# Kernel optimization log

Measured on AMD Instinct MI355X. Metric: run time of the kernel, lower is better.

Reference implementation:

```python
import jax, jax.numpy as jnp
import numpy as np

DIM = 2048
N_HEADS = 16
HEAD_DIM = DIM // N_HEADS  # 128
HIDDEN = 8192
EPS = 1e-6
NEG = -1e9


def rmsnorm(x, w):
    xf = x.astype(jnp.float32)
    y = xf * jax.lax.rsqrt(jnp.mean(xf * xf, axis=-1, keepdims=True) + EPS)
    return y.astype(x.dtype) * w


def apply_rope(x, cos, sin):
    # x: [B,S,H,Hd]; cos/sin: [S,Hd//2] -> broadcast [1,S,1,Hd//2]
    xf = x.astype(jnp.float32)
    xr = xf[..., 0::2]
    xi = xf[..., 1::2]
    c = cos[None, :, None, :]
    s = sin[None, :, None, :]
    or_ = xr * c - xi * s
    oi_ = xr * s + xi * c
    out = jnp.stack([or_, oi_], axis=-1).reshape(x.shape)
    return out.astype(x.dtype)


def setup_inputs() -> dict:
    key = jax.random.key(0)
    ks = jax.random.split(key, 10)
    B, S = 1, 2048
    x = jax.random.normal(ks[0], (B, S, DIM), dtype=jnp.float32)
    # RoPE frequencies (Llama-style, theta=10000)
    inv_freq = 1.0 / (10000.0 ** (jnp.arange(0, HEAD_DIM, 2, dtype=jnp.float32) / HEAD_DIM))
    angles = jnp.arange(S, dtype=jnp.float32)[:, None] * inv_freq[None, :]  # [S, Hd//2]
    freqs_cos = jnp.cos(angles)
    freqs_sin = jnp.sin(angles)
    # causal additive mask [1,1,S,S]
    mask = jnp.where(jnp.tril(jnp.ones((S, S), dtype=bool)), 0.0, NEG).astype(jnp.float32)[None, None]
    sc = 0.02
    wq = jax.random.normal(ks[1], (DIM, DIM), dtype=jnp.float32) * sc
    wk = jax.random.normal(ks[2], (DIM, DIM), dtype=jnp.float32) * sc
    wv = jax.random.normal(ks[3], (DIM, DIM), dtype=jnp.float32) * sc
    wo = jax.random.normal(ks[4], (DIM, DIM), dtype=jnp.float32) * sc
    w1 = jax.random.normal(ks[5], (DIM, HIDDEN), dtype=jnp.float32) * sc
    w2 = jax.random.normal(ks[6], (HIDDEN, DIM), dtype=jnp.float32) * sc
    w3 = jax.random.normal(ks[7], (DIM, HIDDEN), dtype=jnp.float32) * sc
    attn_norm_w = jnp.ones((DIM,), dtype=jnp.float32)
    ffn_norm_w = jnp.ones((DIM,), dtype=jnp.float32)
    return {"x": x, "freqs_cos": freqs_cos, "freqs_sin": freqs_sin, "mask": mask,
            "wq": wq, "wk": wk, "wv": wv, "wo": wo, "w1": w1, "w2": w2, "w3": w3,
            "attn_norm_w": attn_norm_w, "ffn_norm_w": ffn_norm_w}


def reference(x, freqs_cos, freqs_sin, mask, wq, wk, wv, wo, w1, w2, w3, attn_norm_w, ffn_norm_w):
    B, S, D = x.shape
    # --- attention (pre-norm) ---
    hn = rmsnorm(x, attn_norm_w)
    q = (hn @ wq).reshape(B, S, N_HEADS, HEAD_DIM)
    k = (hn @ wk).reshape(B, S, N_HEADS, HEAD_DIM)
    v = (hn @ wv).reshape(B, S, N_HEADS, HEAD_DIM)
    q = apply_rope(q, freqs_cos, freqs_sin)
    k = apply_rope(k, freqs_cos, freqs_sin)
    scores = jnp.einsum('bqhd,bkhd->bhqk', q, k) / (HEAD_DIM ** 0.5) + mask
    attn = jax.nn.softmax(scores.astype(jnp.float32), axis=-1).astype(q.dtype)
    ctx = jnp.einsum('bhqk,bkhd->bqhd', attn, v).reshape(B, S, D)
    h = x + ctx @ wo
    # --- SwiGLU FFN (pre-norm) ---
    fn = rmsnorm(h, ffn_norm_w)
    ff = (jax.nn.silu(fn @ w1) * (fn @ w3)) @ w2
    return h + ff
```

## Files before the change

kernel.cpp:

```cpp
#include <hip/hip_runtime.h>
#include <hip/hip_bf16.h>

#define DIM 2048
#define HEAD_DIM 128
#define N_HEADS 16
#define SEQ 2048
#define HID 8192
#define SQKV 6144

typedef short bf16x8 __attribute__((ext_vector_type(8)));
typedef float f32x4 __attribute__((ext_vector_type(4)));
using bf16 = __hip_bfloat16;

#define MFMA16(a, b, c) __builtin_amdgcn_mfma_f32_16x16x32_bf16(a, b, c, 0, 0, 0)

__device__ __forceinline__ unsigned short f2bu(float f) {
    union { bf16 b; unsigned short u; } cv;
    cv.b = __float2bfloat16(f);
    return cv.u;
}
__device__ __forceinline__ float bu2f(unsigned short u) {
    union { unsigned short u; bf16 b; } cv;
    cv.u = u;
    return __bfloat162float(cv.b);
}

__device__ __forceinline__ void gl16(const void* g, void* l) {
    __builtin_amdgcn_global_load_lds(
        (const __attribute__((address_space(1))) unsigned int*)g,
        (__attribute__((address_space(3))) unsigned int*)l, 16, 0, 0);
}

__global__ __launch_bounds__(256) void rmsnorm_bf16_k(
    const float* __restrict__ x, const float* __restrict__ w, bf16* __restrict__ y)
{
    const int row = blockIdx.x;
    const int tid = threadIdx.x;
    const float* xr = x + (size_t)row * DIM;
    float4 v0 = ((const float4*)xr)[tid];
    float4 v1 = ((const float4*)xr)[tid + 256];
    float ss = v0.x*v0.x + v0.y*v0.y + v0.z*v0.z + v0.w*v0.w
             + v1.x*v1.x + v1.y*v1.y + v1.z*v1.z + v1.w*v1.w;
    for (int o = 32; o > 0; o >>= 1) ss += __shfl_down(ss, o);
    __shared__ float red[4];
    if ((tid & 63) == 0) red[tid >> 6] = ss;
    __syncthreads();
    float tot = red[0] + red[1] + red[2] + red[3];
    float r = rsqrtf(tot * (1.0f / DIM) + 1e-6f);
    float4 w0 = ((const float4*)w)[tid];
    float4 w1 = ((const float4*)w)[tid + 256];
    ushort4 o0, o1;
    o0.x = f2bu(v0.x * r * w0.x); o0.y = f2bu(v0.y * r * w0.y);
    o0.z = f2bu(v0.z * r * w0.z); o0.w = f2bu(v0.w * r * w0.w);
    o1.x = f2bu(v1.x * r * w1.x); o1.y = f2bu(v1.y * r * w1.y);
    o1.z = f2bu(v1.z * r * w1.z); o1.w = f2bu(v1.w * r * w1.w);
    ushort4* yr = (ushort4*)(y + (size_t)row * DIM);
    yr[tid] = o0;
    yr[tid + 256] = o1;
}

__global__ __launch_bounds__(256) void rmsnorm4_k(
    const bf16* __restrict__ part, const float* __restrict__ x,
    const float* __restrict__ w, float* __restrict__ hout, bf16* __restrict__ y)
{
    const int row = blockIdx.x;
    const int tid = threadIdx.x;
    const size_t base = (size_t)row * DIM + tid * 8;
    const size_t SP = (size_t)SEQ * DIM;
    float4 a0 = *(const float4*)(x + base);
    float4 a1 = *(const float4*)(x + base + 4);
    bf16x8 p0 = *(const bf16x8*)(part + base);
    bf16x8 p1 = *(const bf16x8*)(part + SP + base);
    bf16x8 p2 = *(const bf16x8*)(part + 2 * SP + base);
    bf16x8 p3 = *(const bf16x8*)(part + 3 * SP + base);
    float r8[8];
    float ss = 0.0f;
#pragma unroll
    for (int e = 0; e < 8; ++e) {
        const float xa = e < 4 ? (&a0.x)[e] : (&a1.x)[e - 4];
        const float v = xa + ((bu2f((unsigned short)p0[e]) + bu2f((unsigned short)p1[e]))
                            + (bu2f((unsigned short)p2[e]) + bu2f((unsigned short)p3[e])));
        r8[e] = v;
        ss += v * v;
    }
    *(float4*)(hout + base)     = make_float4(r8[0], r8[1], r8[2], r8[3]);
    *(float4*)(hout + base + 4) = make_float4(r8[4], r8[5], r8[6], r8[7]);
    for (int o = 32; o > 0; o >>= 1) ss += __shfl_down(ss, o);
    __shared__ float red[4];
    if ((tid & 63) == 0) red[tid >> 6] = ss;
    __syncthreads();
    float tot = red[0] + red[1] + red[2] + red[3];
    float r = rsqrtf(tot * (1.0f / DIM) + 1e-6f);
    float4 w0 = *(const float4*)(w + tid * 8);
    float4 w1 = *(const float4*)(w + tid * 8 + 4);
    bf16x8 o8;
#pragma unroll
    for (int e = 0; e < 8; ++e) {
        const float ww = e < 4 ? (&w0.x)[e] : (&w1.x)[e - 4];
        o8[e] = (short)f2bu(r8[e] * r * ww);
    }
    *(bf16x8*)((unsigned short*)y + base) = o8;
}

__global__ __launch_bounds__(256) void reduce4_k(
    const bf16* __restrict__ part, const float* __restrict__ h, float* __restrict__ out)
{
    const size_t i = ((size_t)blockIdx.x * 256 + threadIdx.x) * 8;
    const size_t SP = (size_t)SEQ * DIM;
    float4 a0 = *(const float4*)(h + i);
    float4 a1 = *(const float4*)(h + i + 4);
    bf16x8 p0 = *(const bf16x8*)(part + i);
    bf16x8 p1 = *(const bf16x8*)(part + SP + i);
    bf16x8 p2 = *(const bf16x8*)(part + 2 * SP + i);
    bf16x8 p3 = *(const bf16x8*)(part + 3 * SP + i);
    float r8[8];
#pragma unroll
    for (int e = 0; e < 8; ++e) {
        const float xa = e < 4 ? (&a0.x)[e] : (&a1.x)[e - 4];
        r8[e] = xa + ((bu2f((unsigned short)p0[e]) + bu2f((unsigned short)p1[e]))
                    + (bu2f((unsigned short)p2[e]) + bu2f((unsigned short)p3[e])));
    }
    *(float4*)(out + i)     = make_float4(r8[0], r8[1], r8[2], r8[3]);
    *(float4*)(out + i + 4) = make_float4(r8[4], r8[5], r8[6], r8[7]);
}

__device__ __forceinline__ void convT64_body(
    const float* __restrict__ in, bf16* __restrict__ out, int R, int C,
    int bx, int by)
{
    __shared__ unsigned short t[64][72];
    const int tid = threadIdx.x;
    const int x0 = bx * 64;
    const int y0 = by * 64;
    const int tx = tid & 15, ty = tid >> 4;
#pragma unroll
    for (int i = 0; i < 4; ++i) {
        const int row = ty + i * 16;
        float4 v = *(const float4*)(in + (size_t)(y0 + row) * C + x0 + tx * 4);
        t[tx * 4 + 0][row] = f2bu(v.x);
        t[tx * 4 + 1][row] = f2bu(v.y);
        t[tx * 4 + 2][row] = f2bu(v.z);
        t[tx * 4 + 3][row] = f2bu(v.w);
    }
    __syncthreads();
    const int rx = tid & 7, cy = tid >> 3;
#pragma unroll
    for (int i = 0; i < 2; ++i) {
        const int c = cy + i * 32;
        bf16x8 v = *(const bf16x8*)&t[c][rx * 8];
        *(bf16x8*)(out + (size_t)(x0 + c) * R + y0 + rx * 8) = v;
    }
}

__global__ __launch_bounds__(256) void convT64_k(
    const float* __restrict__ in, bf16* __restrict__ out, int R, int C)
{
    convT64_body(in, out, R, C, blockIdx.x, blockIdx.y);
}

__global__ __launch_bounds__(256) void convT64q_k(
    const float* __restrict__ wq, const float* __restrict__ wk,
    const float* __restrict__ wv, bf16* __restrict__ out)
{
    const int z = blockIdx.z;
    const float* in = z == 0 ? wq : (z == 1 ? wk : wv);
    convT64_body(in, out + (size_t)z * DIM * DIM, DIM, DIM, blockIdx.x, blockIdx.y);
}

__global__ __launch_bounds__(256) void convT64f_k(
    const float* __restrict__ w1, const float* __restrict__ w3,
    bf16* __restrict__ o1, bf16* __restrict__ o3)
{
    const int z = blockIdx.z;
    convT64_body(z ? w3 : w1, z ? o3 : o1, DIM, HID, blockIdx.x, blockIdx.y);
}

__global__ __launch_bounds__(256) void transpose_bf16_k(
    const bf16* __restrict__ in, int istride, bf16* __restrict__ out)
{
    __shared__ unsigned short t[32][33];
    const int tx = threadIdx.x & 31, ty = threadIdx.x >> 5;
    const int x = blockIdx.x * 32 + tx;
    const int y0 = blockIdx.y * 32;
    const unsigned short* inu = (const unsigned short*)in;
    unsigned short* outu = (unsigned short*)out;
#pragma unroll
    for (int i = 0; i < 4; ++i)
        t[ty + i * 8][tx] = inu[(size_t)(y0 + ty + i * 8) * istride + x];
    __syncthreads();
    const int x2 = blockIdx.y * 32 + tx;
    const int y2 = blockIdx.x * 32;
#pragma unroll
    for (int i = 0; i < 4; ++i)
        outu[(size_t)(y2 + ty + i * 8) * SEQ + x2] = t[tx][ty + i * 8];
}

__global__ __launch_bounds__(256) void rope_qk_k(
    bf16* __restrict__ q, bf16* __restrict__ k,
    const float* __restrict__ cosb, const float* __restrict__ sinb)
{
    const int gid = blockIdx.x * 256 + threadIdx.x;
    const int s = gid >> 10;
    const int p = gid & 1023;
    const int h = p >> 6, j = p & 63;
    const size_t off = (size_t)s * SQKV + h * HEAD_DIM + 2 * j;
    const float c = cosb[s * 64 + j], sn = sinb[s * 64 + j];
    float xr = __bfloat162float(q[off]), xi = __bfloat162float(q[off + 1]);
    q[off]     = __float2bfloat16(xr * c - xi * sn);
    q[off + 1] = __float2bfloat16(xr * sn + xi * c);
    xr = __bfloat162float(k[off]); xi = __bfloat162float(k[off + 1]);
    k[off]     = __float2bfloat16(xr * c - xi * sn);
    k[off + 1] = __float2bfloat16(xr * sn + xi * c);
}

template <int EP>
__global__ __launch_bounds__(512, 1) void gemm256_k(
    const bf16* __restrict__ A, const bf16* __restrict__ Bt, const bf16* __restrict__ Bt2,
    bf16* __restrict__ Cb,
    int M, int N, int K, int gx, int ntile, int Ks)
{
    extern __shared__ char smem[];
    const int t512 = threadIdx.x;
    const int w = t512 >> 6, lane = t512 & 63;
    const int lr = lane & 15, lg = lane >> 4;
    const int wm = w >> 2, wn = w & 3;
    const int bofs = (wn & 1) * 64;
    const int swz = (lr & 7) << 4;

    const int nwg = gridDim.x;
    const int q8 = nwg >> 3, r8 = nwg & 7;
    const int xcd = blockIdx.x & 7, seqq = blockIdx.x >> 3;
    const int wgid = (xcd < r8 ? xcd * (q8 + 1) : r8 * (q8 + 1) + (xcd - r8) * q8) + seqq;
    const int split = wgid / ntile;
    const int tile = wgid % ntile;
    const int grp = tile / (4 * gx), rem = tile % (4 * gx);
    const int m0 = (grp * 4 + (rem & 3)) * 256, n0 = (rem >> 2) * 256;
    const int kb0 = split * Ks;
    const int niter = Ks >> 7;

    const bf16* aS[2][2]; const bf16* bS[2][2];
    int sOff[2];
#pragma unroll
    for (int c = 0; c < 2; ++c) {
        const int s = (c * 512 + t512) * 16;
        const int pp = s ^ (((s >> 7) & 7) << 4);
        const int row = pp >> 7, colE = (pp & 127) >> 1;
        sOff[c] = s;
#pragma unroll
        for (int hs = 0; hs < 2; ++hs) {
            aS[hs][c] = A + (size_t)(m0 + hs * 128 + row) * K + kb0 + colE;
            const int rg = n0 + hs * 128 + row;
            if (EP == 4) {
                const int g = rg >> 4;
                const bf16* src = (g & 1) ? Bt2 : Bt;
                const int j = ((g >> 1) << 4) + (rg & 15);
                bS[hs][c] = src + (size_t)j * K + kb0 + colE;
            } else {
                bS[hs][c] = Bt + (size_t)rg * K + kb0 + colE;
            }
        }
    }
    auto stA = [&](int buf, int kt, int hs) {
        char* base = smem + (buf * 2 + hs) * 16384;
        gl16(aS[hs][0] + (kt << 6), base + sOff[0]);
        gl16(aS[hs][1] + (kt << 6), base + sOff[1]);
    };
    auto stB = [&](int buf, int kt, int hs) {
        char* base = smem + 65536 + (buf * 2 + hs) * 16384;
        gl16(bS[hs][0] + (kt << 6), base + sOff[0]);
        gl16(bS[hs][1] + (kt << 6), base + sOff[1]);
    };

    const char* A0m = smem + (0 * 2 + wm) * 16384;
    const char* A1m = smem + (1 * 2 + wm) * 16384;
    const char* B0m = smem + 65536 + (0 * 2 + (wn >> 1)) * 16384;
    const char* B1m = smem + 65536 + (1 * 2 + (wn >> 1)) * 16384;

    f32x4 acc[8][4] = {};
    bf16x8 bfr[4][2];
    bf16x8 x0, x1, x2, x3;

#define SBAR __builtin_amdgcn_s_barrier()
#define LGKM0 do { asm volatile("s_waitcnt lgkmcnt(0)" ::: "memory"); \
                   __builtin_amdgcn_sched_barrier(0); } while (0)
#define LGKM8 do { asm volatile("s_waitcnt lgkmcnt(8)" ::: "memory"); \
                   __builtin_amdgcn_sched_barrier(0); } while (0)
#define WVM(n) do { asm volatile("s_waitcnt vmcnt(" #n ")" ::: "memory"); \
                    __builtin_amdgcn_sched_barrier(0); } while (0)
#define LDA4(base, mf0) do { \
    x0 = *(const bf16x8*)((base) + (((mf0) * 16 + lr) * 128) + ((lg * 16) ^ swz)); \
    x1 = *(const bf16x8*)((base) + (((mf0) * 16 + lr) * 128) + ((64 + lg * 16) ^ swz)); \
    x2 = *(const bf16x8*)((base) + ((((mf0) + 1) * 16 + lr) * 128) + ((lg * 16) ^ swz)); \
    x3 = *(const bf16x8*)((base) + ((((mf0) + 1) * 16 + lr) * 128) + ((64 + lg * 16) ^ swz)); \
    } while (0)
#define LDB8(base) do { \
    _Pragma("unroll") \
    for (int nf = 0; nf < 4; ++nf) { \
        bfr[nf][0] = *(const bf16x8*)((base) + ((bofs + nf * 16 + lr) * 128) + ((lg * 16) ^ swz)); \
        bfr[nf][1] = *(const bf16x8*)((base) + ((bofs + nf * 16 + lr) * 128) + ((64 + lg * 16) ^ swz)); \
    } } while (0)
#define MFMA_PH(mf0) do { \
    __builtin_amdgcn_s_setprio(1); \
    _Pragma("unroll") \
    for (int nf = 0; nf < 4; ++nf) { \
        acc[(mf0)][nf]     = MFMA16(x0, bfr[nf][0], acc[(mf0)][nf]); \
        acc[(mf0)][nf]     = MFMA16(x1, bfr[nf][1], acc[(mf0)][nf]); \
        acc[(mf0) + 1][nf] = MFMA16(x2, bfr[nf][0], acc[(mf0) + 1][nf]); \
        acc[(mf0) + 1][nf] = MFMA16(x3, bfr[nf][1], acc[(mf0) + 1][nf]); \
    } \
    __builtin_amdgcn_s_setprio(0); } while (0)

    stB(0, 0, 0); stB(0, 0, 1); stA(0, 0, 0); stA(0, 0, 1);
    stB(1, 1, 0); stB(1, 1, 1);
    WVM(4);
    SBAR;

    for (int t = 0; t < niter; ++t) {
        const bool pf = (t + 1 < niter);
        const int k1 = 2 * t + 1, k2 = 2 * t + 2, k3 = 2 * t + 3;

        LDB8(B0m);
        LDA4(A0m, 0);
        stA(1, k1, 0);
        LGKM8;
        SBAR; LGKM0; MFMA_PH(0); SBAR;
        LDA4(A0m, 2);
        stA(1, k1, 1);
        SBAR; LGKM0; MFMA_PH(2); SBAR;
        LDA4(A0m, 4);
        if (pf) stB(0, k2, 0);
        SBAR; LGKM0; MFMA_PH(4); SBAR;
        if (pf) { WVM(2); } else { WVM(0); }
        LDA4(A0m, 6);
        if (pf) stB(0, k2, 1);
        SBAR; LGKM0; MFMA_PH(6); SBAR;
        LDB8(B1m);
        LDA4(A1m, 0);
        if (pf) stA(0, k2, 0);
        LGKM8;
        SBAR; LGKM0; MFMA_PH(0); SBAR;
        LDA4(A1m, 2);
        if (pf) stA(0, k2, 1);
        SBAR; LGKM0; MFMA_PH(2); SBAR;
        LDA4(A1m, 4);
        if (pf) stB(1, k3, 0);
        SBAR; LGKM0; MFMA_PH(4); SBAR;
        if (pf) WVM(2);
        LDA4(A1m, 6);
        if (pf) stB(1, k3, 1);
        SBAR; LGKM0; MFMA_PH(6); SBAR;
    }
#undef SBAR
#undef LGKM0
#undef LGKM8
#undef WVM
#undef LDA4
#undef LDB8
#undef MFMA_PH

    if (EP == 4) {
        const int jb = (n0 >> 1) + wn * 32;
        const int NH = N >> 1;
#pragma unroll
        for (int mf = 0; mf < 8; ++mf)
#pragma unroll
            for (int pp = 0; pp < 4; pp += 2) {
                const int row = m0 + wm * 128 + mf * 16 + lg * 4;
                const int j = jb + (pp >> 1) * 16 + lr;
#pragma unroll
                for (int r = 0; r < 4; ++r) {
                    const float a = acc[mf][pp][r];
                    const float b = acc[mf][pp + 1][r];
                    const float s = a / (1.0f + __expf(-a));
                    Cb[(size_t)(row + r) * NH + j] = __float2bfloat16(s * b);
                }
            }
    } else {
        bf16* cb = (EP == 3) ? Cb + (size_t)split * M * N : Cb;
#pragma unroll
        for (int mf = 0; mf < 8; ++mf)
#pragma unroll
            for (int nf = 0; nf < 4; ++nf) {
                const int row = m0 + wm * 128 + mf * 16 + lg * 4;
                const int col = n0 + wn * 64 + nf * 16 + lr;
#pragma unroll
                for (int r = 0; r < 4; ++r)
                    cb[(size_t)(row + r) * N + col] = __float2bfloat16(acc[mf][nf][r]);
            }
    }
}

__global__ __launch_bounds__(512) void attn_fwd_k(
    const bf16* __restrict__ qkv, const bf16* __restrict__ vT, bf16* __restrict__ ctx)
{
    const int tid = threadIdx.x;
    const int w8 = tid >> 6, lane = tid & 63;
    const int lr = lane & 15, lg = lane >> 4;
    const int w = w8 & 3, tsel = w8 >> 2;
    const int h = blockIdx.y;
    const int bx = blockIdx.x;
    const int qidx = tsel ? (31 - bx) : bx;
    const int q0b = qidx * 64;
    const int myNt = qidx + 1;
    const int nt = 32 - bx;

    __shared__ __align__(16) unsigned short Kt[2][64 * 128];
    __shared__ __align__(16) unsigned short Vt[128 * 64];
    __shared__ __align__(16) unsigned short Pp[8][16 * 64];

    const char* kbase = (const char*)(qkv + DIM + h * HEAD_DIM);
    const char* vbase = (const char*)(vT + (size_t)h * HEAD_DIM * SEQ);

    const int krow_c = tid >> 4;
    const int kcolB  = (tid & 15) * 16;
    const int vrow_c = tid >> 3;
    const int vcolB  = (tid & 7) * 16;

    auto stageK = [&](int buf, int kb) {
#pragma unroll
        for (int c = 0; c < 2; ++c) {
            const int r = c * 32 + krow_c;
            gl16(kbase + (size_t)(kb + r) * (SQKV * 2) + (kcolB ^ ((r & 7) << 4)),
                 &Kt[buf][c * 4096 + tid * 8]);
        }
    };
    auto stageV = [&](int kb) {
#pragma unroll
        for (int c = 0; c < 2; ++c) {
            const int r = c * 64 + vrow_c;
            gl16(vbase + (size_t)r * (SEQ * 2) + kb * 2 + (vcolB ^ ((r & 7) << 4)),
                 &Vt[c * 4096 + tid * 8]);
        }
    };

    bf16x8 qf[4];
    const bf16* qrow = qkv + (size_t)(q0b + w * 16 + lr) * SQKV + h * HEAD_DIM;
#pragma unroll
    for (int dt = 0; dt < 4; ++dt)
        qf[dt] = *(const bf16x8*)(qrow + dt * 32 + lg * 8);

    f32x4 o[8] = {};
    float m[4], l[4];
#pragma unroll
    for (int j = 0; j < 4; ++j) { m[j] = -3e38f; l[j] = 0.0f; }
    const float scale = 0.08838834764831845f;

    stageK(0, 0);
    asm volatile("s_waitcnt vmcnt(0)" ::: "memory");
    __builtin_amdgcn_sched_barrier(0);
    __builtin_amdgcn_s_barrier();

    int cur = 0;
    for (int t = 0; t < nt; ++t) {
        const int kb = t * 64;
        const bool pf = (t + 1 < nt);
        stageV(kb);
        if (pf) stageK(cur ^ 1, kb + 64);
        const bool act = (t < myNt);

        if (act) {
            f32x4 s[4] = {};
            __builtin_amdgcn_s_setprio(1);
#pragma unroll
            for (int ss = 0; ss < 4; ++ss) {
                const int r = ss * 16 + lr;
                const int sw = (r & 7) << 3;
#pragma unroll
                for (int dt = 0; dt < 4; ++dt) {
                    bf16x8 kf = *(const bf16x8*)&Kt[cur][r * 128 + ((dt * 32 + lg * 8) ^ sw)];
                    s[ss] = MFMA16(qf[dt], kf, s[ss]);
                }
            }
            __builtin_amdgcn_s_setprio(0);

            float al[4];
#pragma unroll
            for (int j = 0; j < 4; ++j) {
                const int qi = q0b + w * 16 + lg * 4 + j;
                const int prow = lg * 4 + j;
                const int psw = (prow & 7) << 3;
                float a[4];
#pragma unroll
                for (int ss = 0; ss < 4; ++ss)
                    a[ss] = s[ss][j] * scale + ((kb + ss * 16 + lr) > qi ? -1e9f : 0.0f);
                float mx = fmaxf(fmaxf(a[0], a[1]), fmaxf(a[2], a[3]));
                mx = fmaxf(mx, __shfl_xor(mx, 1));
                mx = fmaxf(mx, __shfl_xor(mx, 2));
                mx = fmaxf(mx, __shfl_xor(mx, 4));
                mx = fmaxf(mx, __shfl_xor(mx, 8));
                const float mn = fmaxf(m[j], mx);
                const float asc = __expf(m[j] - mn);
                float e0 = __expf(a[0] - mn), e1 = __expf(a[1] - mn);
                float e2 = __expf(a[2] - mn), e3 = __expf(a[3] - mn);
                float rs = (e0 + e1) + (e2 + e3);
                rs += __shfl_xor(rs, 1); rs += __shfl_xor(rs, 2);
                rs += __shfl_xor(rs, 4); rs += __shfl_xor(rs, 8);
                l[j] = l[j] * asc + rs;
                m[j] = mn;
                al[j] = asc;
                Pp[w8][prow * 64 + ((lr)      ^ psw)] = f2bu(e0);
                Pp[w8][prow * 64 + ((16 + lr) ^ psw)] = f2bu(e1);
                Pp[w8][prow * 64 + ((32 + lr) ^ psw)] = f2bu(e2);
                Pp[w8][prow * 64 + ((48 + lr) ^ psw)] = f2bu(e3);
            }
#pragma unroll
            for (int d2 = 0; d2 < 8; ++d2)
#pragma unroll
                for (int j = 0; j < 4; ++j) o[d2][j] *= al[j];
        }

        if (pf) { asm volatile("s_waitcnt vmcnt(2)" ::: "memory"); }
        else    { asm volatile("s_waitcnt vmcnt(0)" ::: "memory"); }
        __builtin_amdgcn_sched_barrier(0);
        __builtin_amdgcn_s_barrier();

        if (act) {
            asm volatile("s_waitcnt lgkmcnt(0)" ::: "memory");
            __builtin_amdgcn_sched_barrier(0);
            const int asw = (lr & 7) << 3;
            bf16x8 pa0 = *(const bf16x8*)&Pp[w8][lr * 64 + ((lg * 8)      ^ asw)];
            bf16x8 pa1 = *(const bf16x8*)&Pp[w8][lr * 64 + ((32 + lg * 8) ^ asw)];

            __builtin_amdgcn_s_setprio(1);
#pragma unroll
            for (int d2 = 0; d2 < 8; ++d2) {
                const int rv = d2 * 16 + lr;
                const int vsw = (rv & 7) << 3;
                bf16x8 vf0 = *(const bf16x8*)&Vt[rv * 64 + ((lg * 8)      ^ vsw)];
                bf16x8 vf1 = *(const bf16x8*)&Vt[rv * 64 + ((32 + lg * 8) ^ vsw)];
                o[d2] = MFMA16(pa0, vf0, o[d2]);
                o[d2] = MFMA16(pa1, vf1, o[d2]);
            }
            __builtin_amdgcn_s_setprio(0);
        }

        __builtin_amdgcn_s_barrier();
        cur ^= 1;
    }

#pragma unroll
    for (int j = 0; j < 4; ++j) {
        const float inv = 1.0f / l[j];
        bf16* dst = ctx + (size_t)(q0b + w * 16 + lg * 4 + j) * DIM + h * HEAD_DIM + lr;
#pragma unroll
        for (int d2 = 0; d2 < 8; ++d2)
            dst[d2 * 16] = __float2bfloat16(o[d2][j] * inv);
    }
}

extern "C" void kernel_launch(void* const* d_in, const int* in_sizes, int n_in,
                              void* d_out, int out_size, void* d_ws, size_t ws_size,
                              hipStream_t stream)
{
    const float* x   = (const float*)d_in[0];
    const float* fc  = (const float*)d_in[1];
    const float* fs  = (const float*)d_in[2];
    const float* wq  = (const float*)d_in[4];
    const float* wk  = (const float*)d_in[5];
    const float* wv  = (const float*)d_in[6];
    const float* wo  = (const float*)d_in[7];
    const float* w1  = (const float*)d_in[8];
    const float* w2  = (const float*)d_in[9];
    const float* w3  = (const float*)d_in[10];
    const float* anw = (const float*)d_in[11];
    const float* fnw = (const float*)d_in[12];
    float* out = (float*)d_out;

    char* p = (char*)d_ws;
    auto alloc = [&](size_t n) { char* r = p; p += (n + 255) & ~(size_t)255; return r; };
    bf16* wT  = (bf16*)alloc((size_t)HID * DIM * 2);
    bf16* hn  = (bf16*)alloc((size_t)SEQ * DIM * 2);
    bf16* qkv = (bf16*)alloc((size_t)SEQ * SQKV * 2);
    bf16* vt  = (bf16*)alloc((size_t)SEQ * DIM * 2);
    bf16* ctx = (bf16*)alloc((size_t)SEQ * DIM * 2);
    bf16* fn  = (bf16*)alloc((size_t)SEQ * DIM * 2);
    float* h  = (float*)alloc((size_t)SEQ * DIM * 4);
    bf16* g   = (bf16*)alloc((size_t)SEQ * HID * 2);
    bf16* sk  = (bf16*)alloc((size_t)4 * SEQ * DIM * 2);
    bf16* w3T = hn;

    const int LDS256 = 131072;
    (void)hipFuncSetAttribute((const void*)gemm256_k<0>,
        hipFuncAttributeMaxDynamicSharedMemorySize, LDS256);
    (void)hipFuncSetAttribute((const void*)gemm256_k<3>,
        hipFuncAttributeMaxDynamicSharedMemorySize, LDS256);
    (void)hipFuncSetAttribute((const void*)gemm256_k<4>,
        hipFuncAttributeMaxDynamicSharedMemorySize, LDS256);

    rmsnorm_bf16_k<<<SEQ, 256, 0, stream>>>(x, anw, hn);

    convT64q_k<<<dim3(DIM / 64, DIM / 64, 3), 256, 0, stream>>>(wq, wk, wv, wT);
    gemm256_k<0><<<(SEQ / 256) * (SQKV / 256), 512, LDS256, stream>>>(
        hn, wT, nullptr, qkv, SEQ, SQKV, DIM, SQKV / 256, (SEQ / 256) * (SQKV / 256), DIM);

    rope_qk_k<<<(SEQ * 1024) / 256, 256, 0, stream>>>(qkv, qkv + DIM, fc, fs);
    transpose_bf16_k<<<dim3(DIM / 32, SEQ / 32), 256, 0, stream>>>(qkv + 2 * DIM, SQKV, vt);

    attn_fwd_k<<<dim3(16, N_HEADS), 512, 0, stream>>>(qkv, vt, ctx);

    convT64_k<<<dim3(DIM / 64, DIM / 64), 256, 0, stream>>>(wo, wT, DIM, DIM);
    gemm256_k<3><<<(SEQ / 256) * (DIM / 256) * 4, 512, LDS256, stream>>>(
        ctx, wT, nullptr, sk, SEQ, DIM, DIM, DIM / 256, (SEQ / 256) * (DIM / 256), 512);
    rmsnorm4_k<<<SEQ, 256, 0, stream>>>(sk, x, fnw, h, fn);

    convT64f_k<<<dim3(HID / 64, DIM / 64, 2), 256, 0, stream>>>(w1, w3, wT, w3T);
    gemm256_k<4><<<(SEQ / 256) * ((2 * HID) / 256), 512, LDS256, stream>>>(
        fn, wT, w3T, g, SEQ, 2 * HID, DIM, (2 * HID) / 256,
        (SEQ / 256) * ((2 * HID) / 256), DIM);

    convT64_k<<<dim3(DIM / 64, HID / 64), 256, 0, stream>>>(w2, wT, HID, DIM);
    gemm256_k<3><<<(SEQ / 256) * (DIM / 256) * 4, 512, LDS256, stream>>>(
        g, wT, nullptr, sk, SEQ, DIM, HID, DIM / 256, (SEQ / 256) * (DIM / 256), 2048);
    reduce4_k<<<(SEQ * DIM / 8) / 256, 256, 0, stream>>>(sk, h, out);
}
```

Measured before the change: 448.3 us.

## Switch GEMM inner loop to 32x32x16 MFMA and vectorize RoPE kernel

The main GEMM kernel moves from 16x16x32 MFMA tiles to 32x32x16 MFMA tiles. The LDS fragment loads, accumulator layout and both epilogues are rewritten to match, and the SwiGLU epilogue now pairs gate and up values through a lane shuffle. Larger MFMA tiles need fewer LDS reads per FLOP and fewer instructions, at the cost of a different register layout and more scattered stores in the epilogue. The RoPE kernel is also vectorized to handle 8 bf16 elements per thread with 16-byte loads and stores.

```diff
diff --git a/kernel.cpp b/kernel.cpp
--- a/kernel.cpp
+++ b/kernel.cpp
@@ -10,9 +10,11 @@
 
 typedef short bf16x8 __attribute__((ext_vector_type(8)));
 typedef float f32x4 __attribute__((ext_vector_type(4)));
+typedef float f32x16 __attribute__((ext_vector_type(16)));
 using bf16 = __hip_bfloat16;
 
 #define MFMA16(a, b, c) __builtin_amdgcn_mfma_f32_16x16x32_bf16(a, b, c, 0, 0, 0)
+#define MFMA32(a, b, c) __builtin_amdgcn_mfma_f32_32x32x16_bf16(a, b, c, 0, 0, 0)
 
 __device__ __forceinline__ unsigned short f2bu(float f) {
     union { bf16 b; unsigned short u; } cv;
@@ -200,17 +202,27 @@
     const float* __restrict__ cosb, const float* __restrict__ sinb)
 {
     const int gid = blockIdx.x * 256 + threadIdx.x;
-    const int s = gid >> 10;
-    const int p = gid & 1023;
-    const int h = p >> 6, j = p & 63;
-    const size_t off = (size_t)s * SQKV + h * HEAD_DIM + 2 * j;
-    const float c = cosb[s * 64 + j], sn = sinb[s * 64 + j];
-    float xr = __bfloat162float(q[off]), xi = __bfloat162float(q[off + 1]);
-    q[off]     = __float2bfloat16(xr * c - xi * sn);
-    q[off + 1] = __float2bfloat16(xr * sn + xi * c);
-    xr = __bfloat162float(k[off]); xi = __bfloat162float(k[off + 1]);
-    k[off]     = __float2bfloat16(xr * c - xi * sn);
-    k[off + 1] = __float2bfloat16(xr * sn + xi * c);
+    const int s = gid >> 8;
+    const int p8 = gid & 255;
+    const size_t off = (size_t)s * SQKV + p8 * 8;
+    const int j0 = ((p8 * 8) & 127) >> 1;
+    float4 c4 = *(const float4*)(cosb + s * 64 + j0);
+    float4 s4 = *(const float4*)(sinb + s * 64 + j0);
+    bf16x8 qv = *(const bf16x8*)((const unsigned short*)q + off);
+    bf16x8 kv = *(const bf16x8*)((const unsigned short*)k + off);
+    bf16x8 qo, ko;
+#pragma unroll
+    for (int e = 0; e < 4; ++e) {
+        const float c = (&c4.x)[e], sn = (&s4.x)[e];
+        float xr = bu2f((unsigned short)qv[2 * e]), xi = bu2f((unsigned short)qv[2 * e + 1]);
+        qo[2 * e]     = (short)f2bu(xr * c - xi * sn);
+        qo[2 * e + 1] = (short)f2bu(xr * sn + xi * c);
+        xr = bu2f((unsigned short)kv[2 * e]); xi = bu2f((unsigned short)kv[2 * e + 1]);
+        ko[2 * e]     = (short)f2bu(xr * c - xi * sn);
+        ko[2 * e + 1] = (short)f2bu(xr * sn + xi * c);
+    }
+    *(bf16x8*)((unsigned short*)q + off) = qo;
+    *(bf16x8*)((unsigned short*)k + off) = ko;
 }
 
 template <int EP>
@@ -222,10 +234,11 @@
     extern __shared__ char smem[];
     const int t512 = threadIdx.x;
     const int w = t512 >> 6, lane = t512 & 63;
-    const int lr = lane & 15, lg = lane >> 4;
+    const int l31 = lane & 31, kh = lane >> 5;
     const int wm = w >> 2, wn = w & 3;
     const int bofs = (wn & 1) * 64;
-    const int swz = (lr & 7) << 4;
+    const int swz = (l31 & 7) << 4;
+    const int cb0 = kh * 16;
 
     const int nwg = gridDim.x;
     const int q8 = nwg >> 3, r8 = nwg & 7;
@@ -276,38 +289,41 @@
     const char* B0m = smem + 65536 + (0 * 2 + (wn >> 1)) * 16384;
     const char* B1m = smem + 65536 + (1 * 2 + (wn >> 1)) * 16384;
 
-    f32x4 acc[8][4] = {};
-    bf16x8 bfr[4][2];
-    bf16x8 x0, x1, x2, x3;
+    f32x16 acc[4][2] = {};
+    bf16x8 bfr[2][4];
+    bf16x8 af0, af1, af2, af3;
 
 #define SBAR __builtin_amdgcn_s_barrier()
 #define LGKM0 do { asm volatile("s_waitcnt lgkmcnt(0)" ::: "memory"); \
                    __builtin_amdgcn_sched_barrier(0); } while (0)
-#define LGKM8 do { asm volatile("s_waitcnt lgkmcnt(8)" ::: "memory"); \
-                   __builtin_amdgcn_sched_barrier(0); } while (0)
 #define WVM(n) do { asm volatile("s_waitcnt vmcnt(" #n ")" ::: "memory"); \
                     __builtin_amdgcn_sched_barrier(0); } while (0)
-#define LDA4(base, mf0) do { \
-    x0 = *(const bf16x8*)((base) + (((mf0) * 16 + lr) * 128) + ((lg * 16) ^ swz)); \
-    x1 = *(const bf16x8*)((base) + (((mf0) * 16 + lr) * 128) + ((64 + lg * 16) ^ swz)); \
-    x2 = *(const bf16x8*)((base) + ((((mf0) + 1) * 16 + lr) * 128) + ((lg * 16) ^ swz)); \
-    x3 = *(const bf16x8*)((base) + ((((mf0) + 1) * 16 + lr) * 128) + ((64 + lg * 16) ^ swz)); \
+#define LDA32(base, mf) do { \
+    const char* rb_ = (base) + (((mf) * 32 + l31) * 128); \
+    af0 = *(const bf16x8*)(rb_ + ((cb0 + 0)  ^ swz)); \
+    af1 = *(const bf16x8*)(rb_ + ((cb0 + 32) ^ swz)); \
+    af2 = *(const bf16x8*)(rb_ + ((cb0 + 64) ^ swz)); \
+    af3 = *(const bf16x8*)(rb_ + ((cb0 + 96) ^ swz)); \
     } while (0)
-#define LDB8(base) do { \
+#define LDB32(base) do { \
     _Pragma("unroll") \
-    for (int nf = 0; nf < 4; ++nf) { \
-        bfr[nf][0] = *(const bf16x8*)((base) + ((bofs + nf * 16 + lr) * 128) + ((lg * 16) ^ swz)); \
-        bfr[nf][1] = *(const bf16x8*)((base) + ((bofs + nf * 16 + lr) * 128) + ((64 + lg * 16) ^ swz)); \
+    for (int nf = 0; nf < 2; ++nf) { \
+        const char* rb_ = (base) + ((bofs + nf * 32 + l31) * 128); \
+        bfr[nf][0] = *(const bf16x8*)(rb_ + ((cb0 + 0)  ^ swz)); \
+        bfr[nf][1] = *(const bf16x8*)(rb_ + ((cb0 + 32) ^ swz)); \
+        bfr[nf][2] = *(const bf16x8*)(rb_ + ((cb0 + 64) ^ swz)); \
+        bfr[nf][3] = *(const bf16x8*)(rb_ + ((cb0 + 96) ^ swz)); \
     } } while (0)
-#define MFMA_PH(mf0) do { \
+#define MFMA_PH(mf) do { \
     __builtin_amdgcn_s_setprio(1); \
-    _Pragma("unroll") \
-    for (int nf = 0; nf < 4; ++nf) { \
-        acc[(mf0)][nf]     = MFMA16(x0, bfr[nf][0], acc[(mf0)][nf]); \
-        acc[(mf0)][nf]     = MFMA16(x1, bfr[nf][1], acc[(mf0)][nf]); \
-        acc[(mf0) + 1][nf] = MFMA16(x2, bfr[nf][0], acc[(mf0) + 1][nf]); \
-        acc[(mf0) + 1][nf] = MFMA16(x3, bfr[nf][1], acc[(mf0) + 1][nf]); \
-    } \
+    acc[mf][0] = MFMA32(af0, bfr[0][0], acc[mf][0]); \
+    acc[mf][1] = MFMA32(af0, bfr[1][0], acc[mf][1]); \
+    acc[mf][0] = MFMA32(af1, bfr[0][1], acc[mf][0]); \
+    acc[mf][1] = MFMA32(af1, bfr[1][1], acc[mf][1]); \
+    acc[mf][0] = MFMA32(af2, bfr[0][2], acc[mf][0]); \
+    acc[mf][1] = MFMA32(af2, bfr[1][2], acc[mf][1]); \
+    acc[mf][0] = MFMA32(af3, bfr[0][3], acc[mf][0]); \
+    acc[mf][1] = MFMA32(af3, bfr[1][3], acc[mf][1]); \
     __builtin_amdgcn_s_setprio(0); } while (0)
 
     stB(0, 0, 0); stB(0, 0, 1); stA(0, 0, 0); stA(0, 0, 1);
@@ -319,73 +335,74 @@
         const bool pf = (t + 1 < niter);
         const int k1 = 2 * t + 1, k2 = 2 * t + 2, k3 = 2 * t + 3;
 
-        LDB8(B0m);
-        LDA4(A0m, 0);
+        LDB32(B0m);
+        LDA32(A0m, 0);
         stA(1, k1, 0);
-        LGKM8;
         SBAR; LGKM0; MFMA_PH(0); SBAR;
-        LDA4(A0m, 2);
+        LDA32(A0m, 1);
         stA(1, k1, 1);
+        SBAR; LGKM0; MFMA_PH(1); SBAR;
+        LDA32(A0m, 2);
+        if (pf) stB(0, k2, 0);
         SBAR; LGKM0; MFMA_PH(2); SBAR;
-        LDA4(A0m, 4);
-        if (pf) stB(0, k2, 0);
-        SBAR; LGKM0; MFMA_PH(4); SBAR;
         if (pf) { WVM(2); } else { WVM(0); }
-        LDA4(A0m, 6);
+        LDA32(A0m, 3);
         if (pf) stB(0, k2, 1);
-        SBAR; LGKM0; MFMA_PH(6); SBAR;
-        LDB8(B1m);
-        LDA4(A1m, 0);
+        SBAR; LGKM0; MFMA_PH(3); SBAR;
+        LDB32(B1m);
+        LDA32(A1m, 0);
         if (pf) stA(0, k2, 0);
-        LGKM8;
         SBAR; LGKM0; MFMA_PH(0); SBAR;
-        LDA4(A1m, 2);
+        LDA32(A1m, 1);
         if (pf) stA(0, k2, 1);
+        SBAR; LGKM0; MFMA_PH(1); SBAR;
+        LDA32(A1m, 2);
+        if (pf) stB(1, k3, 0);
         SBAR; LGKM0; MFMA_PH(2); SBAR;
-        LDA4(A1m, 4);
-        if (pf) stB(1, k3, 0);
-        SBAR; LGKM0; MFMA_PH(4); SBAR;
         if (pf) WVM(2);
-        LDA4(A1m, 6);
+        LDA32(A1m, 3);
         if (pf) stB(1, k3, 1);
-        SBAR; LGKM0; MFMA_PH(6); SBAR;
+        SBAR; LGKM0; MFMA_PH(3); SBAR;
     }
 #undef SBAR
 #undef LGKM0
-#undef LGKM8
 #undef WVM
-#undef LDA4
-#undef LDB8
+#undef LDA32
+#undef LDB32
 #undef MFMA_PH
 
     if (EP == 4) {
-        const int jb = (n0 >> 1) + wn * 32;
         const int NH = N >> 1;
 #pragma unroll
-        for (int mf = 0; mf < 8; ++mf)
-#pragma unroll
-            for (int pp = 0; pp < 4; pp += 2) {
-                const int row = m0 + wm * 128 + mf * 16 + lg * 4;
-                const int j = jb + (pp >> 1) * 16 + lr;
-#pragma unroll
-                for (int r = 0; r < 4; ++r) {
-                    const float a = acc[mf][pp][r];
-                    const float b = acc[mf][pp + 1][r];
-                    const float s = a / (1.0f + __expf(-a));
-                    Cb[(size_t)(row + r) * NH + j] = __float2bfloat16(s * b);
+        for (int mf = 0; mf < 4; ++mf)
+#pragma unroll
+            for (int nf = 0; nf < 2; ++nf) {
+                const int jb = (((n0 + wn * 64 + nf * 32) >> 5) << 4) + (lane & 15);
+#pragma unroll
+                for (int reg = 0; reg < 16; ++reg) {
+                    const float v = acc[mf][nf][reg];
+                    const float vp = __shfl_xor(v, 16);
+                    if ((lane & 31) < 16) {
+                        const int row = m0 + wm * 128 + mf * 32
+                                      + (reg & 3) + 8 * (reg >> 2) + 4 * kh;
+                        const float s = v / (1.0f + __expf(-v));
+                        Cb[(size_t)row * NH + jb] = __float2bfloat16(s * vp);
+                    }
                 }
             }
     } else {
         bf16* cb = (EP == 3) ? Cb + (size_t)split * M * N : Cb;
 #pragma unroll
-        for (int mf = 0; mf < 8; ++mf)
-#pragma unroll
-            for (int nf = 0; nf < 4; ++nf) {
-                const int row = m0 + wm * 128 + mf * 16 + lg * 4;
-                const int col = n0 + wn * 64 + nf * 16 + lr;
-#pragma unroll
-                for (int r = 0; r < 4; ++r)
-                    cb[(size_t)(row + r) * N + col] = __float2bfloat16(acc[mf][nf][r]);
+        for (int mf = 0; mf < 4; ++mf)
+#pragma unroll
+            for (int nf = 0; nf < 2; ++nf) {
+                const int col = n0 + wn * 64 + nf * 32 + l31;
+#pragma unroll
+                for (int reg = 0; reg < 16; ++reg) {
+                    const int row = m0 + wm * 128 + mf * 32
+                                  + (reg & 3) + 8 * (reg >> 2) + 4 * kh;
+                    cb[(size_t)row * N + col] = __float2bfloat16(acc[mf][nf][reg]);
+                }
             }
     }
 }
@@ -593,7 +610,7 @@
     gemm256_k<0><<<(SEQ / 256) * (SQKV / 256), 512, LDS256, stream>>>(
         hn, wT, nullptr, qkv, SEQ, SQKV, DIM, SQKV / 256, (SEQ / 256) * (SQKV / 256), DIM);
 
-    rope_qk_k<<<(SEQ * 1024) / 256, 256, 0, stream>>>(qkv, qkv + DIM, fc, fs);
+    rope_qk_k<<<(SEQ * 256) / 256, 256, 0, stream>>>(qkv, qkv + DIM, fc, fs);
     transpose_bf16_k<<<dim3(DIM / 32, SEQ / 32), 256, 0, stream>>>(qkv + 2 * DIM, SQKV, vt);
 
     attn_fwd_k<<<dim3(16, N_HEADS), 512, 0, stream>>>(qkv, vt, ctx);
```

Result: slower. 489.3 us (+9.1%).
